# Kernel tuning notes

Hardware: AMD Instinct MI355X
Metric: run time of the kernel (lower is better)

Reference implementation:

```python
import jax, jax.numpy as jnp
import numpy as np

EMBED_DIM = 1024
NUM_HEADS = 8                      # diff-attn heads; effective standard heads = 2*NUM_HEADS
HEAD_DIM = EMBED_DIM // NUM_HEADS // 2   # 64
DEPTH = 12
LAMBDA_INIT = 0.8 - 0.6 * float(np.exp(-0.3 * DEPTH))
RMS_EPS = 1e-5


def _rope_interleaved(x, cos, sin):
    # x: [B,S,H,D]; cos,sin: [S,D//2]. GPT-J style: rotate (even, odd) pairs.
    x1, x2 = x[..., ::2], x[..., 1::2]
    c = cos[None, :, None, :]
    s = sin[None, :, None, :]
    o1 = x1 * c - x2 * s
    o2 = x1 * s + x2 * c
    return jnp.stack([o1, o2], axis=-1).reshape(x.shape)


def _causal_attn(q, k, v, scale):
    # q,k: [B,S,H,D]; v: [B,S,H,Dv] -> out [B,S,H,Dv]
    S = q.shape[1]
    scores = jnp.einsum('bqhd,bkhd->bhqk', q, k) * scale
    causal = jnp.tril(jnp.ones((S, S), dtype=bool))
    scores = jnp.where(causal[None, None], scores, jnp.finfo(scores.dtype).min)
    p = jax.nn.softmax(scores, axis=-1)
    return jnp.einsum('bhqk,bkhd->bqhd', p, v)


def setup_inputs() -> dict:
    key = jax.random.key(0)
    ks = jax.random.split(key, 10)
    B, S, E, D = 1, 2048, EMBED_DIM, HEAD_DIM
    x = jax.random.normal(ks[0], (B, S, E), jnp.float32)
    # real rotary tables, rotary_dim = head_dim = 64 -> cos/sin [S, 32]
    inv_freq = 1.0 / (10000.0 ** (np.arange(0, D, 2, dtype=np.float64) / D))
    freqs = np.outer(np.arange(S, dtype=np.float64), inv_freq)
    cos = jnp.asarray(np.cos(freqs), jnp.float32)
    sin = jnp.asarray(np.sin(freqs), jnp.float32)
    sc = 1.0 / np.sqrt(E)
    wq = jax.random.normal(ks[1], (E, E), jnp.float32) * sc
    wk = jax.random.normal(ks[2], (E, E), jnp.float32) * sc
    wv = jax.random.normal(ks[3], (E, E), jnp.float32) * sc
    wo = jax.random.normal(ks[4], (E, E), jnp.float32) * sc
    lambda_q1 = jax.random.normal(ks[5], (D,), jnp.float32) * 0.1
    lambda_k1 = jax.random.normal(ks[6], (D,), jnp.float32) * 0.1
    lambda_q2 = jax.random.normal(ks[7], (D,), jnp.float32) * 0.1
    lambda_k2 = jax.random.normal(ks[8], (D,), jnp.float32) * 0.1
    subln_weight = jnp.ones((2 * D,), jnp.float32)
    return dict(x=x, cos=cos, sin=sin, wq=wq, wk=wk, wv=wv, wo=wo,
                lambda_q1=lambda_q1, lambda_k1=lambda_k1,
                lambda_q2=lambda_q2, lambda_k2=lambda_k2,
                subln_weight=subln_weight)


def reference(x, cos, sin, wq, wk, wv, wo,
              lambda_q1, lambda_k1, lambda_q2, lambda_k2, subln_weight):
    B, S, E = x.shape
    H, D = NUM_HEADS, HEAD_DIM
    q = (x @ wq).reshape(B, S, 2 * H, D)
    k = (x @ wk).reshape(B, S, 2 * H, D)
    v = (x @ wv).reshape(B, S, H, 2 * D)
    q = _rope_interleaved(q, cos, sin)
    k = _rope_interleaved(k, cos, sin)
    q = q.reshape(B, S, H, 2, D)
    k = k.reshape(B, S, H, 2, D)
    q1, q2 = q[..., 0, :], q[..., 1, :]
    k1, k2 = k[..., 0, :], k[..., 1, :]
    scale = D ** -0.5  # flash_attn default softmax scale
    a1 = _causal_attn(q1, k1, v, scale)  # [B,S,H,2D]
    a2 = _causal_attn(q2, k2, v, scale)
    lam1 = jnp.exp(jnp.sum(lambda_q1 * lambda_k1))
    lam2 = jnp.exp(jnp.sum(lambda_q2 * lambda_k2))
    lam_full = lam1 - lam2 + LAMBDA_INIT
    attn = a1 - lam_full * a2
    # sublayer RMSNorm over 2*head_dim, computed in fp32
    ms = jnp.mean(jnp.square(attn.astype(jnp.float32)), axis=-1, keepdims=True)
    attn = (attn.astype(jnp.float32) * jax.lax.rsqrt(ms + RMS_EPS)).astype(attn.dtype)
    attn = attn * subln_weight
    attn = attn * (1.0 - LAMBDA_INIT)
    attn = attn.reshape(B, S, E)
    return attn @ wo
```

## Files before the change

### kernel.cpp

```cpp
#include <hip/hip_runtime.h>
#include <hip/hip_bf16.h>

#define SEQ 2048
#define EMB 1024
#define NH 8
#define HD 64
#define DVH 128
#define LAMBDA_INIT 0.7836057665316245f
#define ONE_MINUS_LI 0.2163942334683755f
#define RMS_EPS 1e-5f
#define QK_SCALE 0.18033688011112042f

typedef __attribute__((ext_vector_type(8))) short short8_t;
typedef __attribute__((ext_vector_type(4))) float f32x4;

__device__ __forceinline__ short f2bf(float f) {
    __hip_bfloat16 h = __float2bfloat16(f);
    return *reinterpret_cast<short*>(&h);
}
__device__ __forceinline__ float bf2f(short s) {
    unsigned u = ((unsigned)(unsigned short)s) << 16;
    return __uint_as_float(u);
}
__device__ __forceinline__ float fast_exp2(float x) {
    float r;
    asm("v_exp_f32 %0, %1" : "=v"(r) : "v"(x));
    return r;
}
__device__ __forceinline__ void gload16(const void* g, void* l) {
    __builtin_amdgcn_global_load_lds((const __attribute__((address_space(1))) unsigned int*)g,
                                     (__attribute__((address_space(3))) unsigned int*)l, 16, 0, 0);
}

__global__ __launch_bounds__(256) void k_prep(const float* __restrict__ x, short* __restrict__ xb,
                                              const float* __restrict__ w0, const float* __restrict__ w1,
                                              const float* __restrict__ w2, const float* __restrict__ w3,
                                              short* __restrict__ o0, short* __restrict__ o1,
                                              short* __restrict__ o2, short* __restrict__ o3,
                                              const float* __restrict__ lq1, const float* __restrict__ lk1,
                                              const float* __restrict__ lq2, const float* __restrict__ lk2,
                                              float* __restrict__ lam) {
    const int bid = blockIdx.x;
    const int tid = threadIdx.x;
    if (bid < 2048) {
        int i = bid * 256 + tid;
        const float4* xv = (const float4*)x;
        float4 v = xv[i];
        short4 r = make_short4(f2bf(v.x), f2bf(v.y), f2bf(v.z), f2bf(v.w));
        *(short4*)(xb + i * 4) = r;
    } else if (bid < 3072) {
        int t = bid - 2048;
        int bz = t >> 8, by = (t >> 4) & 15, bx = t & 15;
        const float* w = bz == 0 ? w0 : bz == 1 ? w1 : bz == 2 ? w2 : w3;
        short* o = bz == 0 ? o0 : bz == 1 ? o1 : bz == 2 ? o2 : o3;
        __shared__ float tbuf[64][65];
        int r0 = by * 64, c0 = bx * 64;
        int col = tid & 63, rb = tid >> 6;
#pragma unroll
        for (int i = 0; i < 16; i++) {
            int row = rb + i * 4;
            tbuf[row][col] = w[(r0 + row) * EMB + c0 + col];
        }
        __syncthreads();
#pragma unroll
        for (int i = 0; i < 16; i++) {
            int fr = rb + i * 4;
            o[(c0 + fr) * EMB + r0 + col] = f2bf(tbuf[col][fr]);
        }
    } else {
        if (tid < 64) {
            float p1 = lq1[tid] * lk1[tid], p2 = lq2[tid] * lk2[tid];
#pragma unroll
            for (int off = 32; off >= 1; off >>= 1) {
                p1 += __shfl_xor(p1, off);
                p2 += __shfl_xor(p2, off);
            }
            if (tid == 0) lam[0] = expf(p1) - expf(p2) + LAMBDA_INIT;
        }
    }
}

template <int MI, int NI, int OUTM>
__global__ __launch_bounds__(256) void k_gemm(const short* __restrict__ A,
                                              const short* __restrict__ B0,
                                              const short* __restrict__ B1,
                                              const short* __restrict__ B2,
                                              const float* __restrict__ cosT,
                                              const float* __restrict__ sinT,
                                              short* __restrict__ Cq, short* __restrict__ Ktl,
                                              short* __restrict__ Vtl, float* __restrict__ Cf) {
    constexpr int BM = MI * 32, BN = NI * 32, BK = 64;
    constexpr int STAGE_SZ = (BM + BN) * BK;
    constexpr int SH_EPI = (OUTM == 0) ? BM * 136 : 0;
    constexpr int SHSZ = (2 * STAGE_SZ > SH_EPI) ? 2 * STAGE_SZ : SH_EPI;
    __shared__ short SH[SHSZ];
    const int bn = blockIdx.x * BN;
    const int bm = blockIdx.y * BM;
    const int nsel = bn >> 10;
    const int nloc = bn & 1023;
    const short* Bt = nsel == 0 ? B0 : (nsel == 1 ? B1 : B2);
    const int tid = threadIdx.x;
    const int w = tid >> 6, l = tid & 63;
    const int lr = l & 15, lg = l >> 4;
    const int wm = (w >> 1) * (MI * 16), wn = (w & 1) * (NI * 16);
    const int lrow8 = l >> 3, lchunk = l & 7;
    const int schunk = (lchunk ^ lrow8) * 8;

    f32x4 acc[MI][NI];
#pragma unroll
    for (int mi = 0; mi < MI; mi++)
#pragma unroll
        for (int ni = 0; ni < NI; ni++) acc[mi][ni] = f32x4{0.f, 0.f, 0.f, 0.f};

#define STAGEIT(BUF, K0)                                                                      \
    {                                                                                         \
        short* Ab_ = SH + (BUF) * STAGE_SZ;                                                   \
        short* Bb_ = Ab_ + BM * BK;                                                           \
        _Pragma("unroll") for (int j = 0; j < BM / 32; j++) {                                 \
            int r0 = w * (BM / 4) + j * 8;                                                    \
            gload16(A + (size_t)(bm + r0 + lrow8) * EMB + (K0) + schunk, &Ab_[r0 * BK]);      \
        }                                                                                     \
        _Pragma("unroll") for (int j = 0; j < BN / 32; j++) {                                 \
            int r0 = w * (BN / 4) + j * 8;                                                    \
            gload16(Bt + (size_t)(nloc + r0 + lrow8) * EMB + (K0) + schunk, &Bb_[r0 * BK]);   \
        }                                                                                     \
    }

    STAGEIT(0, 0);
    __syncthreads();
#pragma unroll 1
    for (int t = 0; t < EMB / BK; ++t) {
        const int cur = t & 1;
        if (t + 1 < EMB / BK) STAGEIT(cur ^ 1, (t + 1) * BK);
        const short* Ab_ = SH + cur * STAGE_SZ;
        const short* Bb_ = Ab_ + BM * BK;
#pragma unroll
        for (int kk = 0; kk < 2; kk++) {
            const int pcs = (((kk << 2) + lg) ^ (lr & 7)) << 3;
            short8_t af[MI], bf[NI];
#pragma unroll
            for (int mi = 0; mi < MI; mi++)
                af[mi] = *(const short8_t*)&Ab_[(wm + mi * 16 + lr) * BK + pcs];
#pragma unroll
            for (int ni = 0; ni < NI; ni++)
                bf[ni] = *(const short8_t*)&Bb_[(wn + ni * 16 + lr) * BK + pcs];
#pragma unroll
            for (int mi = 0; mi < MI; mi++)
#pragma unroll
                for (int ni = 0; ni < NI; ni++)
                    acc[mi][ni] =
                        __builtin_amdgcn_mfma_f32_16x16x32_bf16(af[mi], bf[ni], acc[mi][ni], 0, 0, 0);
        }
        __syncthreads();
    }
#undef STAGEIT

    if (OUTM == 1) {
#pragma unroll
        for (int mi = 0; mi < MI; mi++)
#pragma unroll
            for (int ni = 0; ni < NI; ni++)
#pragma unroll
                for (int r = 0; r < 4; r++) {
                    int row = bm + wm + mi * 16 + lg * 4 + r;
                    int col = wn + ni * 16 + lr;
                    Cf[row * EMB + bn + col] = acc[mi][ni][r];
                }
        return;
    }
    const int hh = nloc >> 7;
    short* tile = SH;
    if (nsel < 2) {
#pragma unroll
        for (int mi = 0; mi < MI; mi++)
#pragma unroll
            for (int ni = 0; ni < NI; ni++) {
                const int c = wn + ni * 16 + lr;
                const int p = (c & 63) >> 1;
#pragma unroll
                for (int r = 0; r < 4; r++) {
                    const int row = wm + mi * 16 + lg * 4 + r;
                    const int grow = bm + row;
                    float v = acc[mi][ni][r];
                    float partner = __shfl_xor(v, 1);
                    float cs = cosT[grow * 32 + p], sn = sinT[grow * 32 + p];
                    float out = (lr & 1) ? (partner * sn + v * cs) : (v * cs - partner * sn);
                    if (nsel == 0)
                        Cq[((size_t)hh << 18) + (size_t)grow * 128 + c] = f2bf(out * QK_SCALE);
                    else
                        tile[row * 136 + c] = f2bf(out);
                }
            }
        if (nsel == 1) {
            __syncthreads();
            const int kb0 = blockIdx.y * (BM / 32);
#pragma unroll
            for (int i = 0; i < BM / 16; i++) {
                int flat = tid + i * 256;
                int kbi = flat >> 9, rest = flat & 511;
                int slot = rest >> 6, ln = rest & 63;
                int lqq = ln & 15;
                int comp = slot >> 2, tt = (slot >> 1) & 1, s = slot & 1;
                int lgg = ln >> 4;
                int row = kbi * 32 + tt * 16 + lqq;
                int fb = comp * 64 + s * 32 + lgg * 8;
                short8_t v = *(const short8_t*)&tile[row * 136 + fb];
                *(short8_t*)(Ktl + ((size_t)(hh * 64 + kb0 + kbi) * 8 + slot) * 512 + ln * 8) = v;
            }
        }
    } else {
#pragma unroll
        for (int mi = 0; mi < MI; mi++)
#pragma unroll
            for (int ni = 0; ni < NI; ni++) {
                const int c = wn + ni * 16 + lr;
#pragma unroll
                for (int r = 0; r < 4; r++) {
                    const int row = wm + mi * 16 + lg * 4 + r;
                    tile[row * 136 + c] = f2bf(acc[mi][ni][r]);
                }
            }
        __syncthreads();
        const int kb0 = blockIdx.y * (BM / 32);
#pragma unroll
        for (int i = 0; i < BM / 16; i++) {
            int flat = tid + i * 256;
            int kbi = flat >> 9, rest = flat & 511;
            int dt = rest >> 6, ln = rest & 63;
            int lgg = ln >> 4, lqq = ln & 15;
            short8_t v;
#pragma unroll
            for (int j = 0; j < 8; j++)
                v[j] = tile[(kbi * 32 + 16 * (j >> 2) + 4 * lgg + (j & 3)) * 136 + dt * 16 + lqq];
            *(short8_t*)(Vtl + ((size_t)(hh * 64 + kb0 + kbi) * 8 + dt) * 512 + ln * 8) = v;
        }
    }
}

__global__ __launch_bounds__(512, 2) void k_attn(const short* __restrict__ Qh,
                                                 const short* __restrict__ Ktl,
                                                 const short* __restrict__ Vtl,
                                                 const float* __restrict__ lamp,
                                                 const float* __restrict__ subln,
                                                 short* __restrict__ Ab) {
    const int bid = blockIdx.x;
    const int h = bid & 7;
    const int tile = 63 - (bid >> 3);
    const int q0 = tile * 32;
    const int tid = threadIdx.x;
    const int w = tid >> 6, l = tid & 63;
    const int lq = l & 15, lg = l >> 4;
    const int comp = w >> 2, ks = w & 3;

    __shared__ __align__(16) float buf[2][2][16][132];
    __shared__ float LBp[2][4][16];

    const int nb = tile + 1;

    short8_t qf0[2], qf1[2];
    {
        const short* qp = Qh + ((size_t)h << 18) + (size_t)(q0 + lq) * 128 + (comp << 6) + lg * 8;
        qf0[0] = *(const short8_t*)(qp);
        qf0[1] = *(const short8_t*)(qp + 32);
        qf1[0] = *(const short8_t*)(qp + 16 * 128);
        qf1[1] = *(const short8_t*)(qp + 16 * 128 + 32);
    }
    short8_t vones;
#pragma unroll
    for (int j = 0; j < 8; j++) vones[j] = (short)0x3F80;

    f32x4 zero4 = {0.f, 0.f, 0.f, 0.f};
    f32x4 o0[8], o1[8];
    f32x4 on0 = zero4, on1 = zero4;
#pragma unroll
    for (int dt = 0; dt < 8; dt++) {
        o0[dt] = zero4;
        o1[dt] = zero4;
    }

    short8_t vfA[8], vfB[8];
    short8_t kfA[2][2], kfB[2][2];

#define LOADKV(VF, KF, KB)                                                                  \
    {                                                                                       \
        const short* vtb = Vtl + (size_t)(h * 64 + (KB)) * 4096 + l * 8;                    \
        const short* ktb = Ktl + ((size_t)(h * 64 + (KB)) * 8 + comp * 4) * 512 + l * 8;    \
        _Pragma("unroll") for (int dt = 0; dt < 8; dt++) VF[dt] =                           \
            *(const short8_t*)(vtb + dt * 512);                                             \
        _Pragma("unroll") for (int tt = 0; tt < 2; tt++) {                                  \
            KF[tt][0] = *(const short8_t*)(ktb + (tt * 2) * 512);                           \
            KF[tt][1] = *(const short8_t*)(ktb + (tt * 2 + 1) * 512);                       \
        }                                                                                   \
    }

#define PROC(VF, KF, KB)                                                                     \
    {                                                                                        \
        const int k0p = (KB) * 32;                                                          \
        f32x4 s0[2], s1[2];                                                                  \
        _Pragma("unroll") for (int tt = 0; tt < 2; tt++) {                                   \
            s0[tt] = zero4;                                                                  \
            s0[tt] = __builtin_amdgcn_mfma_f32_16x16x32_bf16(KF[tt][0], qf0[0], s0[tt], 0, 0, 0); \
            s0[tt] = __builtin_amdgcn_mfma_f32_16x16x32_bf16(KF[tt][1], qf0[1], s0[tt], 0, 0, 0); \
            s1[tt] = zero4;                                                                  \
            s1[tt] = __builtin_amdgcn_mfma_f32_16x16x32_bf16(KF[tt][0], qf1[0], s1[tt], 0, 0, 0); \
            s1[tt] = __builtin_amdgcn_mfma_f32_16x16x32_bf16(KF[tt][1], qf1[1], s1[tt], 0, 0, 0); \
        }                                                                                    \
        float p0[8], p1[8];                                                                  \
        _Pragma("unroll") for (int tt = 0; tt < 2; tt++)                                     \
            _Pragma("unroll") for (int r = 0; r < 4; r++) {                                  \
                p0[tt * 4 + r] = s0[tt][r];                                                  \
                p1[tt * 4 + r] = s1[tt][r];                                                  \
            }                                                                                \
        if (k0p + 31 > q0) {                                                                 \
            _Pragma("unroll") for (int tt = 0; tt < 2; tt++)                                 \
                _Pragma("unroll") for (int r = 0; r < 4; r++) {                              \
                    int kk = k0p + tt * 16 + lg * 4 + r;                                     \
                    if (kk > q0 + lq) p0[tt * 4 + r] = -1e30f;                               \
                    if (kk > q0 + 16 + lq) p1[tt * 4 + r] = -1e30f;                          \
                }                                                                            \
        }                                                                                    \
        _Pragma("unroll") for (int i = 0; i < 8; i++) {                                      \
            p0[i] = fast_exp2(p0[i]);                                                        \
            p1[i] = fast_exp2(p1[i]);                                                        \
        }                                                                                    \
        unsigned pu0[4], pu1[4];                                                             \
        _Pragma("unroll") for (int pr = 0; pr < 4; pr++) {                                   \
            float2 f0 = {p0[2 * pr], p0[2 * pr + 1]};                                        \
            float2 f1 = {p1[2 * pr], p1[2 * pr + 1]};                                        \
            __hip_bfloat162 h0 = __float22bfloat162_rn(f0);                                  \
            __hip_bfloat162 h1 = __float22bfloat162_rn(f1);                                  \
            __builtin_memcpy(&pu0[pr], &h0, 4);                                              \
            __builtin_memcpy(&pu1[pr], &h1, 4);                                              \
        }                                                                                    \
        short8_t pa0, pa1;                                                                   \
        __builtin_memcpy(&pa0, pu0, 16);                                                     \
        __builtin_memcpy(&pa1, pu1, 16);                                                     \
        on0 = __builtin_amdgcn_mfma_f32_16x16x32_bf16(pa0, vones, on0, 0, 0, 0);             \
        on1 = __builtin_amdgcn_mfma_f32_16x16x32_bf16(pa1, vones, on1, 0, 0, 0);             \
        _Pragma("unroll") for (int dt = 0; dt < 8; dt++) {                                   \
            o0[dt] = __builtin_amdgcn_mfma_f32_16x16x32_bf16(pa0, VF[dt], o0[dt], 0, 0, 0);  \
            o1[dt] = __builtin_amdgcn_mfma_f32_16x16x32_bf16(pa1, VF[dt], o1[dt], 0, 0, 0);  \
        }                                                                                    \
    }

    if (ks < nb) LOADKV(vfA, kfA, ks);
    for (int kb = ks; kb < nb; kb += 8) {
        const bool hb = (kb + 4) < nb;
        if (hb) LOADKV(vfB, kfB, kb + 4);
        PROC(vfA, kfA, kb);
        if (hb) {
            if (kb + 8 < nb) LOADKV(vfA, kfA, kb + 8);
            PROC(vfB, kfB, kb + 4);
        }
    }
#undef LOADKV
#undef PROC

#pragma unroll 1
    for (int sub = 0; sub < 2; sub++) {
        const f32x4* o = sub ? o1 : o0;
        const f32x4 on = sub ? on1 : on0;
        const int qbase = q0 + sub * 16;
        if (sub) __syncthreads();
        if (lq == 0) {
#pragma unroll
            for (int r = 0; r < 4; r++) LBp[comp][ks][lg * 4 + r] = on[r];
        }
        if (ks >= 2) {
#pragma unroll
            for (int dt = 0; dt < 8; dt++)
#pragma unroll
                for (int r = 0; r < 4; r++) buf[comp][ks - 2][lg * 4 + r][dt * 16 + lq] = o[dt][r];
        }
        __syncthreads();
        f32x4 oacc[8];
        float lacc = 0.f;
        if (ks < 2) {
#pragma unroll
            for (int dt = 0; dt < 8; dt++)
#pragma unroll
                for (int r = 0; r < 4; r++)
                    oacc[dt][r] = o[dt][r] + buf[comp][ks][lg * 4 + r][dt * 16 + lq];
            lacc = LBp[comp][ks][lq] + LBp[comp][ks + 2][lq];
        }
        __syncthreads();
        if (ks == 1) {
#pragma unroll
            for (int dt = 0; dt < 8; dt++)
#pragma unroll
                for (int r = 0; r < 4; r++) buf[comp][0][lg * 4 + r][dt * 16 + lq] = oacc[dt][r];
            if (l < 16) LBp[comp][1][l] = lacc;
        }
        __syncthreads();
        if (ks == 0) {
#pragma unroll
            for (int dt = 0; dt < 8; dt++)
#pragma unroll
                for (int r = 0; r < 4; r++) oacc[dt][r] += buf[comp][0][lg * 4 + r][dt * 16 + lq];
            lacc += LBp[comp][1][lq];
            const float cs = comp ? lamp[0] : 1.f;
            float inv[4];
#pragma unroll
            for (int r = 0; r < 4; r++) inv[r] = cs / __shfl(lacc, lg * 4 + r);
#pragma unroll
            for (int dt = 0; dt < 8; dt++)
#pragma unroll
                for (int r = 0; r < 4; r++)
                    buf[comp][1][lg * 4 + r][dt * 16 + lq] = oacc[dt][r] * inv[r];
        }
        __syncthreads();
        if (tid < 128) {
            const int row = tid >> 3;
            const int c0 = (tid & 7) * 16;
            float a[16], ss = 0.f;
#pragma unroll
            for (int j = 0; j < 16; j++) {
                a[j] = buf[0][1][row][c0 + j] - buf[1][1][row][c0 + j];
                ss += a[j] * a[j];
            }
            ss += __shfl_xor(ss, 1);
            ss += __shfl_xor(ss, 2);
            ss += __shfl_xor(ss, 4);
            const float sc = rsqrtf(ss * (1.0f / 128.0f) + RMS_EPS) * ONE_MINUS_LI;
            short8_t r8;
#pragma unroll
            for (int j = 0; j < 8; j++) r8[j] = f2bf(a[j] * sc * subln[c0 + j]);
            *(short8_t*)(Ab + (size_t)(qbase + row) * EMB + h * DVH + c0) = r8;
#pragma unroll
            for (int j = 0; j < 8; j++) r8[j] = f2bf(a[8 + j] * sc * subln[c0 + 8 + j]);
            *(short8_t*)(Ab + (size_t)(qbase + row) * EMB + h * DVH + c0 + 8) = r8;
        }
    }
}

extern "C" void kernel_launch(void* const* d_in, const int* in_sizes, int n_in,
                              void* d_out, int out_size, void* d_ws, size_t ws_size,
                              hipStream_t stream) {
    const float* x = (const float*)d_in[0];
    const float* cosT = (const float*)d_in[1];
    const float* sinT = (const float*)d_in[2];
    const float* wq = (const float*)d_in[3];
    const float* wk = (const float*)d_in[4];
    const float* wv = (const float*)d_in[5];
    const float* wo = (const float*)d_in[6];
    const float* lq1 = (const float*)d_in[7];
    const float* lk1 = (const float*)d_in[8];
    const float* lq2 = (const float*)d_in[9];
    const float* lk2 = (const float*)d_in[10];
    const float* subln = (const float*)d_in[11];
    float* out = (float*)d_out;
    char* ws = (char*)d_ws;
    const size_t MB = 1 << 20;
    short* xb = (short*)(ws);
    short* wqt = (short*)(ws + 4 * MB);
    short* wkt = (short*)(ws + 6 * MB);
    short* wvt = (short*)(ws + 8 * MB);
    short* wot = (short*)(ws + 10 * MB);
    short* Qh = (short*)(ws + 12 * MB);
    short* Vtl = (short*)(ws + 20 * MB);
    short* Ktl = (short*)(ws + 24 * MB);
    short* Ab = (short*)(ws + 28 * MB);
    float* lam = (float*)(ws + 32 * MB);

    k_prep<<<3073, 256, 0, stream>>>(x, xb, wq, wk, wv, wo, wqt, wkt, wvt, wot, lq1, lk1, lq2,
                                     lk2, lam);
    k_gemm<2, 4, 0><<<dim3(24, 32), 256, 0, stream>>>(xb, wqt, wkt, wvt, cosT, sinT, Qh, Ktl,
                                                      Vtl, nullptr);
    k_attn<<<512, 512, 0, stream>>>(Qh, Ktl, Vtl, lam, subln, Ab);
    k_gemm<2, 2, 1><<<dim3(16, 32), 256, 0, stream>>>(Ab, wot, wot, wot, nullptr, nullptr,
                                                      nullptr, nullptr, nullptr, out);
}
```

Before: 75.21 us.

## Pair short and long causal query tiles per block to balance attention work

Each attention block now handles two query tiles, ta and 63-ta, so every block does about the same amount of causal work, and the grid halves to 256 blocks. Each K/V tile is loaded once and reused for both query tiles. The row-sum MFMA with a ones vector is replaced by scalar accumulation plus cross-lane shuffles. In exchange, the double-buffered K/V prefetch is dropped, register pressure rises from four output accumulators, and 256 blocks may underfill the GPU's compute units.

Measured after the change: 77.58 us. +3.1%, slower.

```diff
diff --git a/kernel.cpp b/kernel.cpp
--- a/kernel.cpp
+++ b/kernel.cpp
@@ -245,8 +245,10 @@
                                                  short* __restrict__ Ab) {
     const int bid = blockIdx.x;
     const int h = bid & 7;
-    const int tile = 63 - (bid >> 3);
-    const int q0 = tile * 32;
+    const int ta = bid >> 3;
+    const int tb = 63 - ta;
+    const int q0a = ta * 32, q0b = tb * 32;
+    const int nba = ta + 1, nbb = tb + 1;
     const int tid = threadIdx.x;
     const int w = tid >> 6, l = tid & 63;
     const int lq = l & 15, lg = l >> 4;
@@ -255,182 +257,167 @@
     __shared__ __align__(16) float buf[2][2][16][132];
     __shared__ float LBp[2][4][16];
 
-    const int nb = tile + 1;
-
-    short8_t qf0[2], qf1[2];
+    short8_t qa0[2], qa1[2], qb0[2], qb1[2];
     {
-        const short* qp = Qh + ((size_t)h << 18) + (size_t)(q0 + lq) * 128 + (comp << 6) + lg * 8;
-        qf0[0] = *(const short8_t*)(qp);
-        qf0[1] = *(const short8_t*)(qp + 32);
-        qf1[0] = *(const short8_t*)(qp + 16 * 128);
-        qf1[1] = *(const short8_t*)(qp + 16 * 128 + 32);
-    }
-    short8_t vones;
-#pragma unroll
-    for (int j = 0; j < 8; j++) vones[j] = (short)0x3F80;
-
+        const short* qpa = Qh + ((size_t)h << 18) + (size_t)(q0a + lq) * 128 + (comp << 6) + lg * 8;
+        qa0[0] = *(const short8_t*)(qpa);
+        qa0[1] = *(const short8_t*)(qpa + 32);
+        qa1[0] = *(const short8_t*)(qpa + 16 * 128);
+        qa1[1] = *(const short8_t*)(qpa + 16 * 128 + 32);
+        const short* qpb = Qh + ((size_t)h << 18) + (size_t)(q0b + lq) * 128 + (comp << 6) + lg * 8;
+        qb0[0] = *(const short8_t*)(qpb);
+        qb0[1] = *(const short8_t*)(qpb + 32);
+        qb1[0] = *(const short8_t*)(qpb + 16 * 128);
+        qb1[1] = *(const short8_t*)(qpb + 16 * 128 + 32);
+    }
     f32x4 zero4 = {0.f, 0.f, 0.f, 0.f};
-    f32x4 o0[8], o1[8];
-    f32x4 on0 = zero4, on1 = zero4;
+    f32x4 oa0[8], oa1[8], ob0[8], ob1[8];
 #pragma unroll
     for (int dt = 0; dt < 8; dt++) {
-        o0[dt] = zero4;
-        o1[dt] = zero4;
-    }
-
-    short8_t vfA[8], vfB[8];
-    short8_t kfA[2][2], kfB[2][2];
-
-#define LOADKV(VF, KF, KB)                                                                  \
-    {                                                                                       \
-        const short* vtb = Vtl + (size_t)(h * 64 + (KB)) * 4096 + l * 8;                    \
-        const short* ktb = Ktl + ((size_t)(h * 64 + (KB)) * 8 + comp * 4) * 512 + l * 8;    \
-        _Pragma("unroll") for (int dt = 0; dt < 8; dt++) VF[dt] =                           \
-            *(const short8_t*)(vtb + dt * 512);                                             \
-        _Pragma("unroll") for (int tt = 0; tt < 2; tt++) {                                  \
-            KF[tt][0] = *(const short8_t*)(ktb + (tt * 2) * 512);                           \
-            KF[tt][1] = *(const short8_t*)(ktb + (tt * 2 + 1) * 512);                       \
-        }                                                                                   \
-    }
-
-#define PROC(VF, KF, KB)                                                                     \
+        oa0[dt] = zero4;
+        oa1[dt] = zero4;
+        ob0[dt] = zero4;
+        ob1[dt] = zero4;
+    }
+    float lsa0 = 0.f, lsa1 = 0.f, lsb0 = 0.f, lsb1 = 0.f;
+
+    short8_t vf[8];
+    short8_t kf[2][2];
+
+#define PROC1(O, LS, QF, QROW, K0P)                                                          \
     {                                                                                        \
-        const int k0p = (KB) * 32;                                                          \
-        f32x4 s0[2], s1[2];                                                                  \
-        _Pragma("unroll") for (int tt = 0; tt < 2; tt++) {                                   \
-            s0[tt] = zero4;                                                                  \
-            s0[tt] = __builtin_amdgcn_mfma_f32_16x16x32_bf16(KF[tt][0], qf0[0], s0[tt], 0, 0, 0); \
-            s0[tt] = __builtin_amdgcn_mfma_f32_16x16x32_bf16(KF[tt][1], qf0[1], s0[tt], 0, 0, 0); \
-            s1[tt] = zero4;                                                                  \
-            s1[tt] = __builtin_amdgcn_mfma_f32_16x16x32_bf16(KF[tt][0], qf1[0], s1[tt], 0, 0, 0); \
-            s1[tt] = __builtin_amdgcn_mfma_f32_16x16x32_bf16(KF[tt][1], qf1[1], s1[tt], 0, 0, 0); \
-        }                                                                                    \
-        float p0[8], p1[8];                                                                  \
+        f32x4 s_[2];                                                                         \
+        s_[0] = zero4;                                                                       \
+        s_[0] = __builtin_amdgcn_mfma_f32_16x16x32_bf16(kf[0][0], QF[0], s_[0], 0, 0, 0);    \
+        s_[0] = __builtin_amdgcn_mfma_f32_16x16x32_bf16(kf[0][1], QF[1], s_[0], 0, 0, 0);    \
+        s_[1] = zero4;                                                                       \
+        s_[1] = __builtin_amdgcn_mfma_f32_16x16x32_bf16(kf[1][0], QF[0], s_[1], 0, 0, 0);    \
+        s_[1] = __builtin_amdgcn_mfma_f32_16x16x32_bf16(kf[1][1], QF[1], s_[1], 0, 0, 0);    \
+        float p_[8];                                                                         \
         _Pragma("unroll") for (int tt = 0; tt < 2; tt++)                                     \
-            _Pragma("unroll") for (int r = 0; r < 4; r++) {                                  \
-                p0[tt * 4 + r] = s0[tt][r];                                                  \
-                p1[tt * 4 + r] = s1[tt][r];                                                  \
-            }                                                                                \
-        if (k0p + 31 > q0) {                                                                 \
+            _Pragma("unroll") for (int r = 0; r < 4; r++) p_[tt * 4 + r] = s_[tt][r];        \
+        if ((K0P) + 31 > (QROW)) {                                                           \
             _Pragma("unroll") for (int tt = 0; tt < 2; tt++)                                 \
                 _Pragma("unroll") for (int r = 0; r < 4; r++) {                              \
-                    int kk = k0p + tt * 16 + lg * 4 + r;                                     \
-                    if (kk > q0 + lq) p0[tt * 4 + r] = -1e30f;                               \
-                    if (kk > q0 + 16 + lq) p1[tt * 4 + r] = -1e30f;                          \
+                    int kk = (K0P) + tt * 16 + lg * 4 + r;                                   \
+                    if (kk > (QROW) + lq) p_[tt * 4 + r] = -1e30f;                           \
                 }                                                                            \
         }                                                                                    \
         _Pragma("unroll") for (int i = 0; i < 8; i++) {                                      \
-            p0[i] = fast_exp2(p0[i]);                                                        \
-            p1[i] = fast_exp2(p1[i]);                                                        \
-        }                                                                                    \
-        unsigned pu0[4], pu1[4];                                                             \
+            p_[i] = fast_exp2(p_[i]);                                                        \
+            LS += p_[i];                                                                     \
+        }                                                                                    \
+        unsigned pu_[4];                                                                     \
         _Pragma("unroll") for (int pr = 0; pr < 4; pr++) {                                   \
-            float2 f0 = {p0[2 * pr], p0[2 * pr + 1]};                                        \
-            float2 f1 = {p1[2 * pr], p1[2 * pr + 1]};                                        \
-            __hip_bfloat162 h0 = __float22bfloat162_rn(f0);                                  \
-            __hip_bfloat162 h1 = __float22bfloat162_rn(f1);                                  \
-            __builtin_memcpy(&pu0[pr], &h0, 4);                                              \
-            __builtin_memcpy(&pu1[pr], &h1, 4);                                              \
-        }                                                                                    \
-        short8_t pa0, pa1;                                                                   \
-        __builtin_memcpy(&pa0, pu0, 16);                                                     \
-        __builtin_memcpy(&pa1, pu1, 16);                                                     \
-        on0 = __builtin_amdgcn_mfma_f32_16x16x32_bf16(pa0, vones, on0, 0, 0, 0);             \
-        on1 = __builtin_amdgcn_mfma_f32_16x16x32_bf16(pa1, vones, on1, 0, 0, 0);             \
-        _Pragma("unroll") for (int dt = 0; dt < 8; dt++) {                                   \
-            o0[dt] = __builtin_amdgcn_mfma_f32_16x16x32_bf16(pa0, VF[dt], o0[dt], 0, 0, 0);  \
-            o1[dt] = __builtin_amdgcn_mfma_f32_16x16x32_bf16(pa1, VF[dt], o1[dt], 0, 0, 0);  \
-        }                                                                                    \
-    }
-
-    if (ks < nb) LOADKV(vfA, kfA, ks);
-    for (int kb = ks; kb < nb; kb += 8) {
-        const bool hb = (kb + 4) < nb;
-        if (hb) LOADKV(vfB, kfB, kb + 4);
-        PROC(vfA, kfA, kb);
-        if (hb) {
-            if (kb + 8 < nb) LOADKV(vfA, kfA, kb + 8);
-            PROC(vfB, kfB, kb + 4);
-        }
-    }
-#undef LOADKV
-#undef PROC
+            float2 f_ = {p_[2 * pr], p_[2 * pr + 1]};                                        \
+            __hip_bfloat162 h_ = __float22bfloat162_rn(f_);                                  \
+            __builtin_memcpy(&pu_[pr], &h_, 4);                                              \
+        }                                                                                    \
+        short8_t pa_;                                                                        \
+        __builtin_memcpy(&pa_, pu_, 16);                                                     \
+        _Pragma("unroll") for (int dt = 0; dt < 8; dt++)                                     \
+            O[dt] = __builtin_amdgcn_mfma_f32_16x16x32_bf16(pa_, vf[dt], O[dt], 0, 0, 0);    \
+    }
 
 #pragma unroll 1
-    for (int sub = 0; sub < 2; sub++) {
-        const f32x4* o = sub ? o1 : o0;
-        const f32x4 on = sub ? on1 : on0;
-        const int qbase = q0 + sub * 16;
-        if (sub) __syncthreads();
-        if (lq == 0) {
-#pragma unroll
-            for (int r = 0; r < 4; r++) LBp[comp][ks][lg * 4 + r] = on[r];
-        }
-        if (ks >= 2) {
-#pragma unroll
-            for (int dt = 0; dt < 8; dt++)
-#pragma unroll
-                for (int r = 0; r < 4; r++) buf[comp][ks - 2][lg * 4 + r][dt * 16 + lq] = o[dt][r];
-        }
-        __syncthreads();
-        f32x4 oacc[8];
-        float lacc = 0.f;
-        if (ks < 2) {
-#pragma unroll
-            for (int dt = 0; dt < 8; dt++)
-#pragma unroll
-                for (int r = 0; r < 4; r++)
-                    oacc[dt][r] = o[dt][r] + buf[comp][ks][lg * 4 + r][dt * 16 + lq];
-            lacc = LBp[comp][ks][lq] + LBp[comp][ks + 2][lq];
-        }
-        __syncthreads();
-        if (ks == 1) {
-#pragma unroll
-            for (int dt = 0; dt < 8; dt++)
-#pragma unroll
-                for (int r = 0; r < 4; r++) buf[comp][0][lg * 4 + r][dt * 16 + lq] = oacc[dt][r];
-            if (l < 16) LBp[comp][1][l] = lacc;
-        }
-        __syncthreads();
-        if (ks == 0) {
-#pragma unroll
-            for (int dt = 0; dt < 8; dt++)
-#pragma unroll
-                for (int r = 0; r < 4; r++) oacc[dt][r] += buf[comp][0][lg * 4 + r][dt * 16 + lq];
-            lacc += LBp[comp][1][lq];
-            const float cs = comp ? lamp[0] : 1.f;
-            float inv[4];
-#pragma unroll
-            for (int r = 0; r < 4; r++) inv[r] = cs / __shfl(lacc, lg * 4 + r);
-#pragma unroll
-            for (int dt = 0; dt < 8; dt++)
-#pragma unroll
-                for (int r = 0; r < 4; r++)
-                    buf[comp][1][lg * 4 + r][dt * 16 + lq] = oacc[dt][r] * inv[r];
-        }
-        __syncthreads();
-        if (tid < 128) {
-            const int row = tid >> 3;
-            const int c0 = (tid & 7) * 16;
-            float a[16], ss = 0.f;
-#pragma unroll
-            for (int j = 0; j < 16; j++) {
-                a[j] = buf[0][1][row][c0 + j] - buf[1][1][row][c0 + j];
-                ss += a[j] * a[j];
+    for (int kb = ks; kb < nbb; kb += 4) {
+        const int k0p = kb * 32;
+        {
+            const short* vtb = Vtl + (size_t)(h * 64 + kb) * 4096 + l * 8;
+            const short* ktb = Ktl + ((size_t)(h * 64 + kb) * 8 + comp * 4) * 512 + l * 8;
+#pragma unroll
+            for (int dt = 0; dt < 8; dt++) vf[dt] = *(const short8_t*)(vtb + dt * 512);
+#pragma unroll
+            for (int tt = 0; tt < 2; tt++) {
+                kf[tt][0] = *(const short8_t*)(ktb + (tt * 2) * 512);
+                kf[tt][1] = *(const short8_t*)(ktb + (tt * 2 + 1) * 512);
             }
-            ss += __shfl_xor(ss, 1);
-            ss += __shfl_xor(ss, 2);
-            ss += __shfl_xor(ss, 4);
-            const float sc = rsqrtf(ss * (1.0f / 128.0f) + RMS_EPS) * ONE_MINUS_LI;
-            short8_t r8;
-#pragma unroll
-            for (int j = 0; j < 8; j++) r8[j] = f2bf(a[j] * sc * subln[c0 + j]);
-            *(short8_t*)(Ab + (size_t)(qbase + row) * EMB + h * DVH + c0) = r8;
-#pragma unroll
-            for (int j = 0; j < 8; j++) r8[j] = f2bf(a[8 + j] * sc * subln[c0 + 8 + j]);
-            *(short8_t*)(Ab + (size_t)(qbase + row) * EMB + h * DVH + c0 + 8) = r8;
-        }
-    }
+        }
+        PROC1(ob0, lsb0, qb0, q0b, k0p);
+        PROC1(ob1, lsb1, qb1, q0b + 16, k0p);
+        if (kb < nba) {
+            PROC1(oa0, lsa0, qa0, q0a, k0p);
+            PROC1(oa1, lsa1, qa1, q0a + 16, k0p);
+        }
+    }
+#undef PROC1
+
+    lsa0 += __shfl_xor(lsa0, 16);
+    lsa0 += __shfl_xor(lsa0, 32);
+    lsa1 += __shfl_xor(lsa1, 16);
+    lsa1 += __shfl_xor(lsa1, 32);
+    lsb0 += __shfl_xor(lsb0, 16);
+    lsb0 += __shfl_xor(lsb0, 32);
+    lsb1 += __shfl_xor(lsb1, 16);
+    lsb1 += __shfl_xor(lsb1, 32);
+
+#define MERGE(O, LS, QBASE)                                                                  \
+    {                                                                                        \
+        if (ks >= 2) {                                                                       \
+            _Pragma("unroll") for (int dt = 0; dt < 8; dt++)                                 \
+                _Pragma("unroll") for (int r = 0; r < 4; r++)                                \
+                    buf[comp][ks - 2][lg * 4 + r][dt * 16 + lq] = O[dt][r];                  \
+            if (l < 16) LBp[comp][ks][l] = LS;                                               \
+        }                                                                                    \
+        __syncthreads();                                                                     \
+        f32x4 oacc_[8];                                                                      \
+        float lacc_ = LS;                                                                    \
+        if (ks < 2) {                                                                        \
+            _Pragma("unroll") for (int dt = 0; dt < 8; dt++)                                 \
+                _Pragma("unroll") for (int r = 0; r < 4; r++)                                \
+                    oacc_[dt][r] = O[dt][r] + buf[comp][ks][lg * 4 + r][dt * 16 + lq];       \
+            lacc_ = LS + LBp[comp][ks + 2][lq];                                              \
+        }                                                                                    \
+        __syncthreads();                                                                     \
+        if (ks == 1) {                                                                       \
+            _Pragma("unroll") for (int dt = 0; dt < 8; dt++)                                 \
+                _Pragma("unroll") for (int r = 0; r < 4; r++)                                \
+                    buf[comp][0][lg * 4 + r][dt * 16 + lq] = oacc_[dt][r];                   \
+            if (l < 16) LBp[comp][1][l] = lacc_;                                             \
+        }                                                                                    \
+        __syncthreads();                                                                     \
+        if (ks == 0) {                                                                       \
+            _Pragma("unroll") for (int dt = 0; dt < 8; dt++)                                 \
+                _Pragma("unroll") for (int r = 0; r < 4; r++)                                \
+                    oacc_[dt][r] += buf[comp][0][lg * 4 + r][dt * 16 + lq];                  \
+            lacc_ += LBp[comp][1][lq];                                                       \
+            const float cs_ = comp ? lamp[0] : 1.f;                                         \
+            float inv_[4];                                                                   \
+            _Pragma("unroll") for (int r = 0; r < 4; r++)                                    \
+                inv_[r] = cs_ / __shfl(lacc_, lg * 4 + r);                                   \
+            _Pragma("unroll") for (int dt = 0; dt < 8; dt++)                                 \
+                _Pragma("unroll") for (int r = 0; r < 4; r++)                                \
+                    buf[comp][1][lg * 4 + r][dt * 16 + lq] = oacc_[dt][r] * inv_[r];         \
+        }                                                                                    \
+        __syncthreads();                                                                     \
+        if (tid < 128) {                                                                     \
+            const int row_ = tid >> 3;                                                       \
+            const int c0_ = (tid & 7) * 16;                                                  \
+            float a_[16], ss_ = 0.f;                                                         \
+            _Pragma("unroll") for (int j = 0; j < 16; j++) {                                 \
+                a_[j] = buf[0][1][row_][c0_ + j] - buf[1][1][row_][c0_ + j];                 \
+                ss_ += a_[j] * a_[j];                                                        \
+            }                                                                                \
+            ss_ += __shfl_xor(ss_, 1);                                                       \
+            ss_ += __shfl_xor(ss_, 2);                                                       \
+            ss_ += __shfl_xor(ss_, 4);                                                       \
+            const float sc_ = rsqrtf(ss_ * (1.0f / 128.0f) + RMS_EPS) * ONE_MINUS_LI;        \
+            short8_t r8_;                                                                    \
+            _Pragma("unroll") for (int j = 0; j < 8; j++)                                    \
+                r8_[j] = f2bf(a_[j] * sc_ * subln[c0_ + j]);                                 \
+            *(short8_t*)(Ab + (size_t)((QBASE) + row_) * EMB + h * DVH + c0_) = r8_;         \
+            _Pragma("unroll") for (int j = 0; j < 8; j++)                                    \
+                r8_[j] = f2bf(a_[8 + j] * sc_ * subln[c0_ + 8 + j]);                         \
+            *(short8_t*)(Ab + (size_t)((QBASE) + row_) * EMB + h * DVH + c0_ + 8) = r8_;     \
+        }                                                                                    \
+        __syncthreads();                                                                     \
+    }
+
+    MERGE(ob0, lsb0, q0b);
+    MERGE(ob1, lsb1, q0b + 16);
+    MERGE(oa0, lsa0, q0a);
+    MERGE(oa1, lsa1, q0a + 16);
+#undef MERGE
 }
 
 extern "C" void kernel_launch(void* const* d_in, const int* in_sizes, int n_in,
@@ -466,7 +453,7 @@
                                      lk2, lam);
     k_gemm<2, 4, 0><<<dim3(24, 32), 256, 0, stream>>>(xb, wqt, wkt, wvt, cosT, sinT, Qh, Ktl,
                                                       Vtl, nullptr);
-    k_attn<<<512, 512, 0, stream>>>(Qh, Ktl, Vtl, lam, subln, Ab);
+    k_attn<<<256, 512, 0, stream>>>(Qh, Ktl, Vtl, lam, subln, Ab);
     k_gemm<2, 2, 1><<<dim3(16, 32), 256, 0, stream>>>(Ab, wot, wot, wot, nullptr, nullptr,
                                                       nullptr, nullptr, nullptr, out);
 }
```
